# Kernel tuning notes

Measured on AMD Instinct MI355X. Metric: run time of the kernel, lower is better.

## Reference

```python
import jax, jax.numpy as jnp
import numpy as np
from jax import lax

DIM = 256
PROJ = 128
NPOS = 8          # ceil(log2(2*64+5))
EXT = 64          # attnExtension
NLAYERS = 4
HEADS = 4
KDIM = PROJ + NPOS
EPS = 1e-5


def _ln(x):
    # LayerNorm over last dim, no affine (elementwise_affine=False)
    mu = jnp.mean(x, axis=-1, keepdims=True)
    var = jnp.mean(jnp.square(x - mu), axis=-1, keepdims=True)
    return (x - mu) * lax.rsqrt(var + EPS)


def setup_inputs() -> dict:
    key = jax.random.key(0)
    ks = jax.random.split(key, 18)
    L = 2048
    s = 0.05
    return {
        "input": jax.random.normal(ks[0], (L, PROJ), jnp.float32),
        "residual": jax.random.normal(ks[1], (5 * L, DIM), jnp.float32),
        "W_proj": jax.random.normal(ks[2], (5 * DIM, KDIM), jnp.float32) * s,
        "b_proj": jnp.zeros((5 * DIM,), jnp.float32),
        "Wq": jax.random.normal(ks[3], (DIM, DIM), jnp.float32) * s,
        "bq": jnp.zeros((DIM,), jnp.float32),
        "Wk": jax.random.normal(ks[4], (DIM, KDIM), jnp.float32) * s,
        "bk": jnp.zeros((DIM,), jnp.float32),
        "Wv": jax.random.normal(ks[5], (DIM, KDIM), jnp.float32) * s,
        "bv": jnp.zeros((DIM,), jnp.float32),
        "Wo": jax.random.normal(ks[6], (DIM, DIM), jnp.float32) * s,
        "bo": jnp.zeros((DIM,), jnp.float32),
        "conv_w": jax.random.normal(ks[7], (NLAYERS, DIM, DIM, 3), jnp.float32) * s,
        "conv_b": jnp.zeros((NLAYERS, DIM), jnp.float32),
        "W_skip": jax.random.normal(ks[8], (DIM, DIM), jnp.float32) * s,
        "b_skip": jnp.zeros((DIM,), jnp.float32),
    }


def reference(input, residual, W_proj, b_proj, Wq, bq, Wk, bk, Wv, bv,
              Wo, bo, conv_w, conv_b, W_skip, b_skip):
    L = input.shape[0]
    T = 5 * L  # tgt length
    hd = DIM // HEADS

    # positional embeddings: pos[:, i] = (arange(L) % 2^(i+1)) / 2^i
    n = jnp.arange(L, dtype=input.dtype)[:, None]
    i = jnp.arange(NPOS, dtype=input.dtype)[None, :]
    pos = jnp.mod(n, 2.0 ** (i + 1.0)) / (2.0 ** i)

    src = jnp.concatenate([input, pos], axis=1)            # (L, KDIM)
    tgt = (src @ W_proj.T + b_proj).reshape(T, DIM)        # (5L, DIM)

    # banded mask: row j may attend col i iff 5i-EXT <= j < 5i+5+EXT
    j = jnp.arange(T)[:, None]
    ii = jnp.arange(L)[None, :]
    d = j - 5 * ii
    allowed = (d >= -EXT) & (d < 5 + EXT)                  # (5L, L)

    # multihead attention (eval mode, dropout skipped)
    q = (tgt @ Wq.T + bq).reshape(T, HEADS, hd).transpose(1, 0, 2)
    k = (src @ Wk.T + bk).reshape(L, HEADS, hd).transpose(1, 0, 2)
    v = (src @ Wv.T + bv).reshape(L, HEADS, hd).transpose(1, 0, 2)
    scores = jnp.einsum('hqd,hkd->hqk', q, k) / jnp.sqrt(jnp.asarray(hd, q.dtype))
    scores = jnp.where(allowed[None], scores, -jnp.inf)
    attn = jax.nn.softmax(scores, axis=-1)
    ctx = jnp.einsum('hqk,hkd->hqd', attn, v).transpose(1, 0, 2).reshape(T, DIM)
    attn_out = ctx @ Wo.T + bo

    cnn_in = _ln(attn_out) + residual                      # (5L, DIM)

    # spectral-norm conv stack (weights assumed pre-normalized) + tanh
    x = cnn_in.T[None]                                     # (1, DIM, 5L)
    for l in range(NLAYERS):
        x = jnp.tanh(
            lax.conv_general_dilated(x, conv_w[l], window_strides=(1,),
                                     padding=[(1, 1)])
            + conv_b[l][None, :, None])
    cnn_out = x[0].T                                       # (5L, DIM)

    return _ln(cnn_out + cnn_in @ W_skip.T + b_skip)
```

## Files before the change

kernel.cpp:

```cpp
#include <hip/hip_runtime.h>
#include <hip/hip_bf16.h>

#define PROJ 128
#define KPAD 192
#define EPS 1e-5f

typedef __attribute__((ext_vector_type(4))) float f32x4;
typedef __attribute__((ext_vector_type(8))) short bf16x8;
typedef __attribute__((ext_vector_type(4))) unsigned int u32x4;

__device__ inline float bflo(unsigned u){ union{unsigned x;float f;}c; c.x = u<<16; return c.f; }
__device__ inline float bfhi(unsigned u){ union{unsigned x;float f;}c; c.x = u & 0xffff0000u; return c.f; }
__device__ inline float bf2f(unsigned short u){ union{unsigned x;float f;}c; c.x = ((unsigned)u)<<16; return c.f; }
__device__ inline unsigned short f2bf(float f){
    union{float f; unsigned u;} c; c.f = f;
    unsigned r = c.u + 0x7fff + ((c.u >> 16) & 1);
    return (unsigned short)(r >> 16);
}

__global__ __launch_bounds__(256) void prep_all(
    const float* __restrict__ W_proj, const float* __restrict__ Wq,
    const float* __restrict__ Wk, const float* __restrict__ Wv,
    const float* __restrict__ Wo, const float* __restrict__ Ws,
    const float* __restrict__ convw, const float* __restrict__ input,
    const float* __restrict__ bq, const float* __restrict__ b_proj,
    unsigned short* __restrict__ Wqb, unsigned short* __restrict__ Wkb,
    unsigned short* __restrict__ Wvb, unsigned short* __restrict__ Wob,
    unsigned short* __restrict__ Wsb, unsigned short* __restrict__ Wcb,
    unsigned short* __restrict__ WpbT, unsigned short* __restrict__ srcb,
    unsigned short* __restrict__ cinp, float* __restrict__ zbias,
    float* __restrict__ bqc, int L, int T)
{
    int idx = blockIdx.x * 256 + threadIdx.x;
    if (idx < 65536) { Wqb[idx] = f2bf(Wq[idx]); return; }
    idx -= 65536;
    if (idx < 49152) {
        int r = idx / 192, c = idx % 192;
        Wkb[idx] = (c < 136) ? f2bf(Wk[(size_t)r * 136 + c]) : (unsigned short)0;
        return;
    }
    idx -= 49152;
    if (idx < 49152) {
        int r = idx / 192, c = idx % 192;
        Wvb[idx] = (c < 136) ? f2bf(Wv[(size_t)r * 136 + c]) : (unsigned short)0;
        return;
    }
    idx -= 49152;
    if (idx < 65536) { Wob[idx] = f2bf(Wo[idx]); return; }
    idx -= 65536;
    if (idx < 65536) {
        int e = idx & 7;
        int lane = (idx >> 3) & 63;
        int fr = (idx >> 9) & 3;
        int wid = (idx >> 11) & 7;
        int kt = idx >> 14;
        int j = fr >> 1, ks = fr & 1;
        int kq = lane >> 4, rowf = lane & 15;
        int o = wid * 32 + j * 16 + rowf;
        int c = kt * 64 + ks * 32 + kq * 8 + e;
        Wsb[idx] = f2bf(Ws[(size_t)o * 256 + c]);
        return;
    }
    idx -= 65536;
    if (idx < 786432) {
        int e = idx & 7;
        int lane = (idx >> 3) & 63;
        int fr = (idx >> 9) & 3;
        int wid = (idx >> 11) & 7;
        int ktl = idx >> 14;
        int l = ktl / 12, kt = ktl % 12;
        int j = fr >> 1, ks = fr & 1;
        int kq = lane >> 4, rowf = lane & 15;
        int o = wid * 32 + j * 16 + rowf;
        int c = kt * 64 + ks * 32 + kq * 8 + e;
        int ktap = c >> 8, ci = c & 255;
        Wcb[idx] = f2bf(convw[(((size_t)l * 256 + o) * 256 + ci) * 3 + ktap]);
        return;
    }
    idx -= 786432;
    if (idx < 327680) {
        int r = idx >> 16;
        int rem = idx & 65535;
        int c = rem >> 8, d = rem & 255;
        WpbT[idx] = (c < 136) ? f2bf(W_proj[(size_t)(r * 256 + d) * 136 + c])
                              : (unsigned short)0;
        return;
    }
    idx -= 327680;
    if (idx < L * KPAD) {
        int n = idx / KPAD, c = idx % KPAD;
        float v = 0.f;
        if (c < PROJ) v = input[(size_t)n * PROJ + c];
        else if (c < PROJ + 8) {
            int i = c - PROJ;
            int mask = (2 << i) - 1;
            v = (float)(n & mask) / (float)(1 << i);
        }
        srcb[idx] = f2bf(v);
        return;
    }
    idx -= L * KPAD;
    if (idx < 512) {
        int row = idx >> 8, c = idx & 255;
        size_t o = (row == 0) ? (size_t)c : (size_t)(T + 1) * 256 + c;
        cinp[o] = 0;
        return;
    }
    idx -= 512;
    if (idx < 256) { zbias[idx] = 0.f; return; }
    idx -= 256;
    if (idx < 1280) {
        int r = idx >> 8, o = idx & 255;
        float s = bq[o];
        const float* wrow = Wq + (size_t)o * 256;
        const float* bp = b_proj + r * 256;
        for (int c = 0; c < 256; ++c) s += wrow[c] * bp[c];
        bqc[idx] = s;
    }
}

__device__ __forceinline__ void gemm_core_64x128(
    unsigned short (&As)[64][72], unsigned short (&Bs)[128][72],
    const unsigned short* __restrict__ A, int lda,
    const unsigned short* __restrict__ B, int ldb,
    const float* __restrict__ bias,
    unsigned short* __restrict__ C, int ldc,
    int K, int m0, int n0)
{
    const int tid = threadIdx.x;
    const int lane = tid & 63;
    const int wid = tid >> 6;
    const int wm = wid >> 1, wn = wid & 1;

    const int ar = tid >> 2, asg = tid & 3;
    const int br = tid >> 1, bsg = tid & 1;

    const unsigned short* Ap = A + (size_t)(m0 + ar) * lda + asg * 16;
    const unsigned short* Bp = B + (size_t)(n0 + br) * ldb + bsg * 32;

    u32x4 ra0, ra1, rb0, rb1, rb2, rb3;
    auto loadregs = [&](int k0) {
        ra0 = *(const u32x4*)(Ap + k0);
        ra1 = *(const u32x4*)(Ap + k0 + 8);
        rb0 = *(const u32x4*)(Bp + k0);
        rb1 = *(const u32x4*)(Bp + k0 + 8);
        rb2 = *(const u32x4*)(Bp + k0 + 16);
        rb3 = *(const u32x4*)(Bp + k0 + 24);
    };
    auto stlds = [&]() {
        *(u32x4*)&As[ar][asg * 16]      = ra0;
        *(u32x4*)&As[ar][asg * 16 + 8]  = ra1;
        *(u32x4*)&Bs[br][bsg * 32]      = rb0;
        *(u32x4*)&Bs[br][bsg * 32 + 8]  = rb1;
        *(u32x4*)&Bs[br][bsg * 32 + 16] = rb2;
        *(u32x4*)&Bs[br][bsg * 32 + 24] = rb3;
    };

    f32x4 acc[2][4];
    #pragma unroll
    for (int i = 0; i < 2; ++i)
        #pragma unroll
        for (int j = 0; j < 4; ++j) acc[i][j] = (f32x4){0.f, 0.f, 0.f, 0.f};

    loadregs(0);
    stlds();
    __syncthreads();

    const int rowf = lane & 15, kb = lane >> 4;
    const int ktiles = K >> 6;
    for (int kt = 0; kt < ktiles; ++kt) {
        if (kt + 1 < ktiles) loadregs((kt + 1) << 6);
        #pragma unroll
        for (int ks = 0; ks < 2; ++ks) {
            bf16x8 af[2], bfr[4];
            #pragma unroll
            for (int i = 0; i < 2; ++i)
                af[i] = *(const bf16x8*)&As[wm * 32 + i * 16 + rowf][ks * 32 + kb * 8];
            #pragma unroll
            for (int j = 0; j < 4; ++j)
                bfr[j] = *(const bf16x8*)&Bs[wn * 64 + j * 16 + rowf][ks * 32 + kb * 8];
            #pragma unroll
            for (int i = 0; i < 2; ++i)
                #pragma unroll
                for (int j = 0; j < 4; ++j)
                    acc[i][j] = __builtin_amdgcn_mfma_f32_16x16x32_bf16(af[i], bfr[j], acc[i][j], 0, 0, 0);
        }
        __syncthreads();
        if (kt + 1 < ktiles) { stlds(); __syncthreads(); }
    }

    const int rq = lane >> 4;
    #pragma unroll
    for (int i = 0; i < 2; ++i) {
        int gm = m0 + wm * 32 + i * 16 + rq * 4;
        #pragma unroll
        for (int j = 0; j < 4; ++j) {
            int gn = n0 + wn * 64 + j * 16 + rowf;
            float bv = bias[gn];
            #pragma unroll
            for (int r = 0; r < 4; ++r)
                C[(size_t)(gm + r) * ldc + gn] = f2bf(acc[i][j][r] + bv);
        }
    }
}

__global__ __launch_bounds__(256) void combine_wq(
    const unsigned short* __restrict__ Wqb,
    const unsigned short* __restrict__ WpbT,
    const float* __restrict__ zbias,
    unsigned short* __restrict__ Wqpb)
{
    __shared__ unsigned short As[64][72];
    __shared__ unsigned short Bs[128][72];
    int bi = blockIdx.x;
    int r = bi >> 3, rem = bi & 7;
    int m0 = (rem >> 1) * 64, n0 = (rem & 1) * 128;
    gemm_core_64x128(As, Bs, Wqb, 256, WpbT + (size_t)r * 65536, 256, zbias,
                     Wqpb + (size_t)r * 65536, 256, 256, m0, n0);
}

__global__ __launch_bounds__(256) void qkv_fused(
    const unsigned short* __restrict__ srcb,
    const unsigned short* __restrict__ Wqpb,
    const unsigned short* __restrict__ Wkb,
    const unsigned short* __restrict__ Wvb,
    const float* __restrict__ bqc, const float* __restrict__ bk,
    const float* __restrict__ bv,
    unsigned short* __restrict__ qb, unsigned short* __restrict__ kb,
    unsigned short* __restrict__ vb)
{
    __shared__ unsigned short As[64][72];
    __shared__ unsigned short Bs[128][72];
    int bi = blockIdx.x;
    const unsigned short *B;
    const float* bias;
    unsigned short* C;
    int ldb, K, m0, n0, ldc;
    if (bi < 320) {
        B = Wqpb; bias = bqc; C = qb; ldb = 256; K = 192; ldc = 1280;
        m0 = (bi / 10) * 64; n0 = (bi % 10) * 128;
    } else if (bi < 384) {
        int t = bi - 320;
        B = Wkb; bias = bk; C = kb; ldb = 192; K = 192; ldc = 256;
        m0 = (t >> 1) * 64; n0 = (t & 1) * 128;
    } else {
        int t = bi - 384;
        B = Wvb; bias = bv; C = vb; ldb = 192; K = 192; ldc = 256;
        m0 = (t >> 1) * 64; n0 = (t & 1) * 128;
    }
    gemm_core_64x128(As, Bs, srcb, KPAD, B, ldb, bias, C, ldc, K, m0, n0);
}

__global__ __launch_bounds__(512) void gemm_ln0(
    const unsigned short* __restrict__ A, int lda,
    const unsigned short* __restrict__ B,
    const float* __restrict__ bias,
    const float* __restrict__ residual,
    unsigned short* __restrict__ out_bf)
{
    __shared__ unsigned short As[64][72];
    __shared__ unsigned short Bs[256][72];
    __shared__ float redS[64][4];
    __shared__ float redQ[64][4];

    const int tid = threadIdx.x;
    const int lane = tid & 63;
    const int wid = tid >> 6;
    const int wm = wid >> 2, wn = wid & 3;
    const int m0 = blockIdx.x * 64;

    const int arow = tid >> 3, acol = (tid & 7) * 8;
    const int brow = tid >> 1, bcol = (tid & 1) * 32;
    const unsigned short* Ap = A + (size_t)(m0 + arow) * lda + acol;
    const unsigned short* Bp = B + (size_t)brow * 256 + bcol;

    u32x4 ra, rb0, rb1, rb2, rb3;
    auto loadregs = [&](int k0) {
        ra  = *(const u32x4*)(Ap + k0);
        rb0 = *(const u32x4*)(Bp + k0);
        rb1 = *(const u32x4*)(Bp + k0 + 8);
        rb2 = *(const u32x4*)(Bp + k0 + 16);
        rb3 = *(const u32x4*)(Bp + k0 + 24);
    };
    auto stlds = [&]() {
        *(u32x4*)&As[arow][acol]       = ra;
        *(u32x4*)&Bs[brow][bcol]       = rb0;
        *(u32x4*)&Bs[brow][bcol + 8]   = rb1;
        *(u32x4*)&Bs[brow][bcol + 16]  = rb2;
        *(u32x4*)&Bs[brow][bcol + 24]  = rb3;
    };

    f32x4 acc[2][4];
    #pragma unroll
    for (int i = 0; i < 2; ++i)
        #pragma unroll
        for (int j = 0; j < 4; ++j) acc[i][j] = (f32x4){0.f, 0.f, 0.f, 0.f};

    loadregs(0);
    stlds();
    __syncthreads();

    const int rowf = lane & 15, kb = lane >> 4;
    #pragma unroll
    for (int kt = 0; kt < 4; ++kt) {
        if (kt < 3) loadregs((kt + 1) << 6);
        #pragma unroll
        for (int ks = 0; ks < 2; ++ks) {
            bf16x8 af[2], bfr[4];
            #pragma unroll
            for (int i = 0; i < 2; ++i)
                af[i] = *(const bf16x8*)&As[wm * 32 + i * 16 + rowf][ks * 32 + kb * 8];
            #pragma unroll
            for (int j = 0; j < 4; ++j)
                bfr[j] = *(const bf16x8*)&Bs[wn * 64 + j * 16 + rowf][ks * 32 + kb * 8];
            #pragma unroll
            for (int i = 0; i < 2; ++i)
                #pragma unroll
                for (int j = 0; j < 4; ++j)
                    acc[i][j] = __builtin_amdgcn_mfma_f32_16x16x32_bf16(af[i], bfr[j], acc[i][j], 0, 0, 0);
        }
        __syncthreads();
        if (kt < 3) { stlds(); __syncthreads(); }
    }

    const int rq = lane >> 4;
    float val[2][4][4];
    #pragma unroll
    for (int i = 0; i < 2; ++i)
        #pragma unroll
        for (int j = 0; j < 4; ++j) {
            int gn = wn * 64 + j * 16 + rowf;
            float bv = bias[gn];
            #pragma unroll
            for (int r = 0; r < 4; ++r) val[i][j][r] = acc[i][j][r] + bv;
        }

    #pragma unroll
    for (int i = 0; i < 2; ++i)
        #pragma unroll
        for (int r = 0; r < 4; ++r) {
            float s = val[i][0][r] + val[i][1][r] + val[i][2][r] + val[i][3][r];
            float q = val[i][0][r] * val[i][0][r] + val[i][1][r] * val[i][1][r]
                    + val[i][2][r] * val[i][2][r] + val[i][3][r] * val[i][3][r];
            #pragma unroll
            for (int m = 1; m < 16; m <<= 1) {
                s += __shfl_xor(s, m, 64);
                q += __shfl_xor(q, m, 64);
            }
            if (rowf == 0) {
                int row = wm * 32 + i * 16 + rq * 4 + r;
                redS[row][wn] = s;
                redQ[row][wn] = q;
            }
        }
    __syncthreads();

    #pragma unroll
    for (int i = 0; i < 2; ++i) {
        #pragma unroll
        for (int r = 0; r < 4; ++r) {
            int row = wm * 32 + i * 16 + rq * 4 + r;
            int gm = m0 + row;
            float s = redS[row][0] + redS[row][1] + redS[row][2] + redS[row][3];
            float q = redQ[row][0] + redQ[row][1] + redQ[row][2] + redQ[row][3];
            float mu = s * (1.f / 256.f);
            float var = q * (1.f / 256.f) - mu * mu;
            float rs = rsqrtf(var + EPS);
            #pragma unroll
            for (int j = 0; j < 4; ++j) {
                int gn = wn * 64 + j * 16 + rowf;
                float nv = (val[i][j][r] - mu) * rs + residual[(size_t)gm * 256 + gn];
                out_bf[(size_t)(gm + 1) * 256 + gn] = f2bf(nv);
            }
        }
    }
}

__global__ __launch_bounds__(256) void attn16(
    const unsigned short* __restrict__ q,
    const unsigned short* __restrict__ k,
    const unsigned short* __restrict__ v,
    unsigned short* __restrict__ ctx, int L)
{
    __shared__ unsigned short ksm[30][264];
    __shared__ unsigned short vsm[30][264];
    const int j0 = blockIdx.x * 16;
    const int iblk0 = (j0 >= 68) ? (j0 - 64) / 5 : 0;
    int ihim = (j0 + 79) / 5; if (ihim > L - 1) ihim = L - 1;
    const int NR = ihim - iblk0 + 1;

    for (int e = threadIdx.x; e < 30 * 32; e += 256) {
        int rr = e >> 5, cc = (e & 31) * 8;
        u32x4 kz = {0, 0, 0, 0}, vz = {0, 0, 0, 0};
        if (rr < NR) {
            kz = *(const u32x4*)&k[(size_t)(iblk0 + rr) * 256 + cc];
            vz = *(const u32x4*)&v[(size_t)(iblk0 + rr) * 256 + cc];
        }
        *(u32x4*)&ksm[rr][cc] = kz;
        *(u32x4*)&vsm[rr][cc] = vz;
    }
    __syncthreads();

    const int tid = threadIdx.x;
    const int h = tid >> 6, lane = tid & 63;
    const int qq = lane & 15, p = lane >> 4;
    const int j = j0 + qq;
    const int colb = h * 64 + p * 16;

    float qr[16];
    {
        u32x4 q0 = *(const u32x4*)&q[(size_t)j * 256 + colb];
        u32x4 q1 = *(const u32x4*)&q[(size_t)j * 256 + colb + 8];
        #pragma unroll
        for (int w = 0; w < 4; ++w) {
            qr[2 * w]     = bflo(q0[w]) * 0.125f;
            qr[2 * w + 1] = bfhi(q0[w]) * 0.125f;
            qr[8 + 2 * w]     = bflo(q1[w]) * 0.125f;
            qr[8 + 2 * w + 1] = bfhi(q1[w]) * 0.125f;
        }
    }
    const int ilo = (j >= 68) ? (j - 64) / 5 : 0;
    int ihi = (j + 64) / 5; if (ihi > L - 1) ihi = L - 1;

    float sc[30];
    #pragma unroll
    for (int t = 0; t < 30; ++t) {
        int i = iblk0 + t;
        u32x4 k0 = *(const u32x4*)&ksm[t][colb];
        u32x4 k1 = *(const u32x4*)&ksm[t][colb + 8];
        float s = 0.f;
        #pragma unroll
        for (int w = 0; w < 4; ++w) {
            s += qr[2 * w]     * bflo(k0[w]);
            s += qr[2 * w + 1] * bfhi(k0[w]);
            s += qr[8 + 2 * w]     * bflo(k1[w]);
            s += qr[8 + 2 * w + 1] * bfhi(k1[w]);
        }
        s += __shfl_xor(s, 16, 64);
        s += __shfl_xor(s, 32, 64);
        sc[t] = (i >= ilo && i <= ihi) ? s : -1e30f;
    }
    float mx = -1e30f;
    #pragma unroll
    for (int t = 0; t < 30; ++t) mx = fmaxf(mx, sc[t]);
    float den = 0.f, o[16];
    #pragma unroll
    for (int d = 0; d < 16; ++d) o[d] = 0.f;
    #pragma unroll
    for (int t = 0; t < 30; ++t) {
        float pt = __expf(sc[t] - mx);
        den += pt;
        u32x4 v0 = *(const u32x4*)&vsm[t][colb];
        u32x4 v1 = *(const u32x4*)&vsm[t][colb + 8];
        #pragma unroll
        for (int w = 0; w < 4; ++w) {
            o[2 * w]     += pt * bflo(v0[w]);
            o[2 * w + 1] += pt * bfhi(v0[w]);
            o[8 + 2 * w]     += pt * bflo(v1[w]);
            o[8 + 2 * w + 1] += pt * bfhi(v1[w]);
        }
    }
    float inv = 1.f / den;
    #pragma unroll
    for (int d = 0; d < 16; ++d)
        ctx[(size_t)j * 256 + colb + d] = f2bf(o[d] * inv);
}

#define CVALID 40
template<int NKT, bool ISCONV>
__device__ __forceinline__ void frag_gemm(
    const unsigned short* __restrict__ Wp,
    unsigned short (*actin)[264],
    f32x4 (&acc)[3][2], int wid, int lane)
{
    const int rowf = lane & 15, kq = lane >> 4;
    const unsigned short* base = Wp + wid * 2048 + lane * 8;
    bf16x8 cur0, cur1, cur2, cur3, nxt0, nxt1, nxt2, nxt3;
    cur0 = *(const bf16x8*)(base);
    cur1 = *(const bf16x8*)(base + 512);
    cur2 = *(const bf16x8*)(base + 1024);
    cur3 = *(const bf16x8*)(base + 1536);
    #pragma unroll
    for (int kt = 0; kt < NKT; ++kt) {
        if (kt + 1 < NKT) {
            const unsigned short* nb = base + (kt + 1) * 16384;
            nxt0 = *(const bf16x8*)(nb);
            nxt1 = *(const bf16x8*)(nb + 512);
            nxt2 = *(const bf16x8*)(nb + 1024);
            nxt3 = *(const bf16x8*)(nb + 1536);
        }
        const int dt = ISCONV ? (kt >> 2) : 1;
        const int cb = ISCONV ? ((kt & 3) * 64) : (kt * 64);
        #pragma unroll
        for (int ks = 0; ks < 2; ++ks) {
            bf16x8 a0 = *(const bf16x8*)&actin[rowf + dt][cb + ks * 32 + kq * 8];
            bf16x8 a1 = *(const bf16x8*)&actin[16 + rowf + dt][cb + ks * 32 + kq * 8];
            bf16x8 a2 = *(const bf16x8*)&actin[32 + rowf + dt][cb + ks * 32 + kq * 8];
            bf16x8 w0 = ks ? cur1 : cur0;
            bf16x8 w1 = ks ? cur3 : cur2;
            acc[0][0] = __builtin_amdgcn_mfma_f32_16x16x32_bf16(a0, w0, acc[0][0], 0, 0, 0);
            acc[0][1] = __builtin_amdgcn_mfma_f32_16x16x32_bf16(a0, w1, acc[0][1], 0, 0, 0);
            acc[1][0] = __builtin_amdgcn_mfma_f32_16x16x32_bf16(a1, w0, acc[1][0], 0, 0, 0);
            acc[1][1] = __builtin_amdgcn_mfma_f32_16x16x32_bf16(a1, w1, acc[1][1], 0, 0, 0);
            acc[2][0] = __builtin_amdgcn_mfma_f32_16x16x32_bf16(a2, w0, acc[2][0], 0, 0, 0);
            acc[2][1] = __builtin_amdgcn_mfma_f32_16x16x32_bf16(a2, w1, acc[2][1], 0, 0, 0);
        }
        cur0 = nxt0; cur1 = nxt1; cur2 = nxt2; cur3 = nxt3;
    }
}

__global__ __launch_bounds__(512, 1) void conv_skip_ln(
    const unsigned short* __restrict__ cinp,
    const unsigned short* __restrict__ Wcb,
    const float* __restrict__ conv_b,
    const unsigned short* __restrict__ Wsb,
    const float* __restrict__ b_skip,
    float* __restrict__ out, int T)
{
    __shared__ unsigned short actA[50][264];
    __shared__ unsigned short actB[50][264];
    __shared__ float redS[48][8];
    __shared__ float redQ[48][8];

    const int tid = threadIdx.x;
    const int lane = tid & 63;
    const int wid = tid >> 6;
    const int rowf = lane & 15;
    const int kq = lane >> 4;
    const int t0 = blockIdx.x * CVALID;

    for (int e = tid; e < 50 * 32; e += 512) {
        int b = e >> 5, c = (e & 31) * 8;
        int g = t0 - 5 + b;
        u32x4 z = {0, 0, 0, 0};
        if (g >= -1 && g <= T)
            z = *(const u32x4*)&cinp[(size_t)(g + 1) * 256 + c];
        *(u32x4*)&actA[b][c] = z;
    }
    if (tid < 256) actB[0][tid] = 0; else actB[49][tid - 256] = 0;
    __syncthreads();

    f32x4 skipacc[3][2];
    #pragma unroll
    for (int i = 0; i < 3; ++i)
        #pragma unroll
        for (int j = 0; j < 2; ++j) skipacc[i][j] = (f32x4){0.f, 0.f, 0.f, 0.f};
    frag_gemm<4, false>(Wsb, actA, skipacc, wid, lane);

    const int gn0 = wid * 32 + rowf;
    f32x4 cacc[3][2];
    #pragma unroll 1
    for (int l = 0; l < 4; ++l) {
        #pragma unroll
        for (int i = 0; i < 3; ++i)
            #pragma unroll
            for (int j = 0; j < 2; ++j) cacc[i][j] = (f32x4){0.f, 0.f, 0.f, 0.f};
        unsigned short (*ain)[264]  = (l & 1) ? actB : actA;
        unsigned short (*aout)[264] = (l & 1) ? actA : actB;
        frag_gemm<12, true>(Wcb + (size_t)l * 196608, ain, cacc, wid, lane);

        float b0 = conv_b[l * 256 + gn0];
        float b1 = conv_b[l * 256 + gn0 + 16];
        if (l < 3) {
            #pragma unroll
            for (int i = 0; i < 3; ++i)
                #pragma unroll
                for (int r = 0; r < 4; ++r) {
                    int w = i * 16 + kq * 4 + r;
                    int g = t0 - 4 + w;
                    bool ok = (g >= 0 && g < T);
                    float v0 = cacc[i][0][r] + b0;
                    float v1 = cacc[i][1][r] + b1;
                    v0 = 1.f - 2.f / (__expf(2.f * v0) + 1.f);
                    v1 = 1.f - 2.f / (__expf(2.f * v1) + 1.f);
                    aout[w + 1][gn0]      = ok ? f2bf(v0) : (unsigned short)0;
                    aout[w + 1][gn0 + 16] = ok ? f2bf(v1) : (unsigned short)0;
                }
            if (tid < 256) aout[0][tid] = 0; else aout[49][tid - 256] = 0;
            __syncthreads();
        } else {
            float sb0 = b_skip[gn0], sb1 = b_skip[gn0 + 16];
            #pragma unroll
            for (int i = 0; i < 3; ++i)
                #pragma unroll
                for (int r = 0; r < 4; ++r) {
                    int w = i * 16 + kq * 4 + r;
                    int g = t0 - 4 + w;
                    bool ok = (g >= 0 && g < T);
                    float v0 = cacc[i][0][r] + b0;
                    float v1 = cacc[i][1][r] + b1;
                    v0 = ok ? (1.f - 2.f / (__expf(2.f * v0) + 1.f)) : 0.f;
                    v1 = ok ? (1.f - 2.f / (__expf(2.f * v1) + 1.f)) : 0.f;
                    skipacc[i][0][r] += sb0 + v0;
                    skipacc[i][1][r] += sb1 + v1;
                }
        }
    }

    #pragma unroll
    for (int i = 0; i < 3; ++i)
        #pragma unroll
        for (int r = 0; r < 4; ++r) {
            float a = skipacc[i][0][r], b = skipacc[i][1][r];
            float s = a + b;
            float q = a * a + b * b;
            #pragma unroll
            for (int m = 1; m < 16; m <<= 1) {
                s += __shfl_xor(s, m, 64);
                q += __shfl_xor(q, m, 64);
            }
            if (rowf == 0) {
                int row = i * 16 + kq * 4 + r;
                redS[row][wid] = s;
                redQ[row][wid] = q;
            }
        }
    __syncthreads();

    #pragma unroll
    for (int i = 0; i < 3; ++i)
        #pragma unroll
        for (int r = 0; r < 4; ++r) {
            int row = i * 16 + kq * 4 + r;
            if (row < 4 || row >= 44) continue;
            int g = t0 - 4 + row;
            if (g >= T) continue;
            float s = 0.f, q = 0.f;
            #pragma unroll
            for (int x = 0; x < 8; ++x) { s += redS[row][x]; q += redQ[row][x]; }
            float mu = s * (1.f / 256.f);
            float var = q * (1.f / 256.f) - mu * mu;
            float rs = rsqrtf(var + EPS);
            out[(size_t)g * 256 + gn0]      = (skipacc[i][0][r] - mu) * rs;
            out[(size_t)g * 256 + gn0 + 16] = (skipacc[i][1][r] - mu) * rs;
        }
}

extern "C" void kernel_launch(void* const* d_in, const int* in_sizes, int n_in,
                              void* d_out, int out_size, void* d_ws, size_t ws_size,
                              hipStream_t stream) {
    const float* input    = (const float*)d_in[0];
    const float* residual = (const float*)d_in[1];
    const float* W_proj   = (const float*)d_in[2];
    const float* b_proj   = (const float*)d_in[3];
    const float* Wq       = (const float*)d_in[4];
    const float* bq       = (const float*)d_in[5];
    const float* Wk       = (const float*)d_in[6];
    const float* bk       = (const float*)d_in[7];
    const float* Wv       = (const float*)d_in[8];
    const float* bv       = (const float*)d_in[9];
    const float* Wo       = (const float*)d_in[10];
    const float* bo       = (const float*)d_in[11];
    const float* conv_w   = (const float*)d_in[12];
    const float* conv_b   = (const float*)d_in[13];
    const float* W_skip   = (const float*)d_in[14];
    const float* b_skip   = (const float*)d_in[15];
    float* out = (float*)d_out;

    const int L = in_sizes[0] / PROJ;
    const int T = 5 * L;

    unsigned short* w16 = (unsigned short*)d_ws;
    size_t off = 0;
    auto alloc = [&](size_t n) { unsigned short* p = w16 + off; off += n; return p; };
    unsigned short* Wqb   = alloc(65536);
    unsigned short* Wkb   = alloc(49152);
    unsigned short* Wvb   = alloc(49152);
    unsigned short* Wob   = alloc(65536);
    unsigned short* Wsb   = alloc(65536);
    unsigned short* Wcb   = alloc(786432);
    unsigned short* WpbT  = alloc(327680);
    unsigned short* Wqpb  = alloc(327680);
    unsigned short* srcb  = alloc((size_t)L * KPAD);
    unsigned short* tgtb  = alloc((size_t)T * 256);
    unsigned short* qb    = alloc((size_t)T * 256);
    unsigned short* kb    = alloc((size_t)L * 256);
    unsigned short* vb    = alloc((size_t)L * 256);
    unsigned short* cinp  = alloc((size_t)(T + 2) * 256);
    float* zbias = (float*)alloc(512);
    float* bqc   = (float*)alloc(2560);

    prep_all<<<dim3(7048), 256, 0, stream>>>(
        W_proj, Wq, Wk, Wv, Wo, W_skip, conv_w, input, bq, b_proj,
        Wqb, Wkb, Wvb, Wob, Wsb, Wcb, WpbT, srcb, cinp, zbias, bqc, L, T);

    combine_wq<<<dim3(40), 256, 0, stream>>>(Wqb, WpbT, zbias, Wqpb);

    qkv_fused<<<dim3(448), 256, 0, stream>>>(
        srcb, Wqpb, Wkb, Wvb, bqc, bk, bv, qb, kb, vb);

    attn16<<<dim3(T / 16), 256, 0, stream>>>(qb, kb, vb, tgtb, L);

    gemm_ln0<<<dim3(T / 64), 512, 0, stream>>>(tgtb, 256, Wob, bo, residual, cinp);

    conv_skip_ln<<<dim3(T / CVALID), 512, 0, stream>>>(
        cinp, Wcb, conv_b, Wsb, b_skip, out, T);
}
```

Measured before the change: 99.47 us.

## Hand-schedule weight prefetch with inline asm ping-pong buffers and raise occupancy

```diff
diff --git a/kernel.cpp b/kernel.cpp
--- a/kernel.cpp
+++ b/kernel.cpp
@@ -17,6 +17,7 @@
     unsigned r = c.u + 0x7fff + ((c.u >> 16) & 1);
     return (unsigned short)(r >> 16);
 }
+__device__ __forceinline__ bf16x8 asbf(u32x4 u){ union{u32x4 a; bf16x8 b;} c; c.a = u; return c.b; }
 
 __global__ __launch_bounds__(256) void prep_all(
     const float* __restrict__ W_proj, const float* __restrict__ Wq,
@@ -475,19 +476,29 @@
 {
     const int rowf = lane & 15, kq = lane >> 4;
     const unsigned short* base = Wp + wid * 2048 + lane * 8;
-    bf16x8 cur0, cur1, cur2, cur3, nxt0, nxt1, nxt2, nxt3;
-    cur0 = *(const bf16x8*)(base);
-    cur1 = *(const bf16x8*)(base + 512);
-    cur2 = *(const bf16x8*)(base + 1024);
-    cur3 = *(const bf16x8*)(base + 1536);
-    #pragma unroll
-    for (int kt = 0; kt < NKT; ++kt) {
+    u32x4 A0, A1, A2, A3, B0, B1, B2, B3;
+
+    asm volatile(
+        "global_load_dwordx4 %0, %4, off\n\t"
+        "global_load_dwordx4 %1, %4, off offset:1024\n\t"
+        "global_load_dwordx4 %2, %4, off offset:2048\n\t"
+        "global_load_dwordx4 %3, %4, off offset:3072"
+        : "=&v"(A0), "=&v"(A1), "=&v"(A2), "=&v"(A3)
+        : "v"(base));
+    asm volatile("s_waitcnt vmcnt(0)"
+                 : "+v"(A0), "+v"(A1), "+v"(A2), "+v"(A3));
+
+    auto body = [&](int kt, u32x4& c0, u32x4& c1, u32x4& c2, u32x4& c3,
+                            u32x4& n0, u32x4& n1, u32x4& n2, u32x4& n3) {
         if (kt + 1 < NKT) {
-            const unsigned short* nb = base + (kt + 1) * 16384;
-            nxt0 = *(const bf16x8*)(nb);
-            nxt1 = *(const bf16x8*)(nb + 512);
-            nxt2 = *(const bf16x8*)(nb + 1024);
-            nxt3 = *(const bf16x8*)(nb + 1536);
+            const unsigned short* nb = base + (size_t)(kt + 1) * 16384;
+            asm volatile(
+                "global_load_dwordx4 %0, %4, off\n\t"
+                "global_load_dwordx4 %1, %4, off offset:1024\n\t"
+                "global_load_dwordx4 %2, %4, off offset:2048\n\t"
+                "global_load_dwordx4 %3, %4, off offset:3072"
+                : "=&v"(n0), "=&v"(n1), "=&v"(n2), "=&v"(n3)
+                : "v"(nb));
         }
         const int dt = ISCONV ? (kt >> 2) : 1;
         const int cb = ISCONV ? ((kt & 3) * 64) : (kt * 64);
@@ -496,8 +507,8 @@
             bf16x8 a0 = *(const bf16x8*)&actin[rowf + dt][cb + ks * 32 + kq * 8];
             bf16x8 a1 = *(const bf16x8*)&actin[16 + rowf + dt][cb + ks * 32 + kq * 8];
             bf16x8 a2 = *(const bf16x8*)&actin[32 + rowf + dt][cb + ks * 32 + kq * 8];
-            bf16x8 w0 = ks ? cur1 : cur0;
-            bf16x8 w1 = ks ? cur3 : cur2;
+            bf16x8 w0 = asbf(ks ? c1 : c0);
+            bf16x8 w1 = asbf(ks ? c3 : c2);
             acc[0][0] = __builtin_amdgcn_mfma_f32_16x16x32_bf16(a0, w0, acc[0][0], 0, 0, 0);
             acc[0][1] = __builtin_amdgcn_mfma_f32_16x16x32_bf16(a0, w1, acc[0][1], 0, 0, 0);
             acc[1][0] = __builtin_amdgcn_mfma_f32_16x16x32_bf16(a1, w0, acc[1][0], 0, 0, 0);
@@ -505,11 +516,21 @@
             acc[2][0] = __builtin_amdgcn_mfma_f32_16x16x32_bf16(a2, w0, acc[2][0], 0, 0, 0);
             acc[2][1] = __builtin_amdgcn_mfma_f32_16x16x32_bf16(a2, w1, acc[2][1], 0, 0, 0);
         }
-        cur0 = nxt0; cur1 = nxt1; cur2 = nxt2; cur3 = nxt3;
-    }
-}
-
-__global__ __launch_bounds__(512, 1) void conv_skip_ln(
+        if (kt + 1 < NKT)
+            asm volatile("s_waitcnt vmcnt(0)"
+                         : "+v"(n0), "+v"(n1), "+v"(n2), "+v"(n3));
+    };
+
+    #pragma unroll
+    for (int k2 = 0; k2 < NKT; k2 += 2) {
+        body(k2,     A0, A1, A2, A3, B0, B1, B2, B3);
+        body(k2 + 1, B0, B1, B2, B3, A0, A1, A2, A3);
+    }
+}
+
+__global__ __launch_bounds__(512)
+__attribute__((amdgpu_waves_per_eu(2)))
+void conv_skip_ln(
     const unsigned short* __restrict__ cinp,
     const unsigned short* __restrict__ Wcb,
     const float* __restrict__ conv_b,
```

Measured after the change: 100.00 us. Within noise of the previous version (+0.5%).
